# Performance work log

Measured on AMD Instinct MI355X. Metric: run time of the kernel, lower is better.

## Reference

```python
import jax, jax.numpy as jnp
import numpy as np

B, L, D, H = 2, 2048, 1024, 16
HD = D // H
HID = 4 * D
EPS = 1e-5


def setup_inputs() -> dict:
    key = jax.random.key(0)
    ks = jax.random.split(key, 16)
    s = 0.02
    inp = {
        "x": jax.random.normal(ks[0], (B, L, D), jnp.float32),
        "mask": jnp.triu(jnp.ones((L, L), bool), k=1),  # True above diagonal -> masked
        "wq": jax.random.normal(ks[1], (D, D), jnp.float32) * s,
        "wk": jax.random.normal(ks[2], (D, D), jnp.float32) * s,
        "wv": jax.random.normal(ks[3], (D, D), jnp.float32) * s,
        "wo": jax.random.normal(ks[4], (D, D), jnp.float32) * s,
        "ln1_g": jnp.ones((D,), jnp.float32),
        "ln1_b": jnp.zeros((D,), jnp.float32),
        "ln2_g": jnp.ones((D,), jnp.float32),
        "ln2_b": jnp.zeros((D,), jnp.float32),
        "w1": jax.random.normal(ks[5], (HID, D), jnp.float32) * s,
        "b1": jnp.zeros((HID,), jnp.float32),
        "wg": jax.random.normal(ks[6], (HID, D), jnp.float32) * s,
        "w2": jax.random.normal(ks[7], (D, HID), jnp.float32) * s,
        "b2": jnp.zeros((D,), jnp.float32),
    }
    return inp


def _layernorm(x, g, b):
    mu = jnp.mean(x, axis=-1, keepdims=True)
    var = jnp.mean(jnp.square(x - mu), axis=-1, keepdims=True)
    return (x - mu) * jax.lax.rsqrt(var + EPS) * g + b


def _attention(h, mask, wq, wk, wv, wo):
    b, l, d = h.shape
    scale = HD ** -0.5
    # torch Linear: y = x @ W.T (W is [out, in])
    q = (h @ wq.T).reshape(b, l, H, HD)
    k = (h @ wk.T).reshape(b, l, H, HD)
    v = (h @ wv.T).reshape(b, l, H, HD)
    attn = jnp.einsum("bqhd,bkhd->bhqk", q, k) * scale
    attn = jnp.where(mask[None, None, :, :], -jnp.inf, attn)
    pos_bias = jnp.arange(l, dtype=attn.dtype) * 0.01  # additive bias along key axis
    attn = attn + pos_bias[None, None, None, :]
    attn = jax.nn.softmax(attn, axis=-1)
    out = jnp.einsum("bhqk,bkhd->bqhd", attn, v).reshape(b, l, d)
    return out @ wo.T


def _ffn(h, w1, b1, wg, w2, b2):
    return (jax.nn.silu(h @ w1.T + b1) * (h @ wg.T)) @ w2.T + b2


def reference(x, mask, wq, wk, wv, wo, ln1_g, ln1_b, ln2_g, ln2_b, w1, b1, wg, w2, b2):
    x = x + _attention(_layernorm(x, ln1_g, ln1_b), mask, wq, wk, wv, wo)
    x = x + _ffn(_layernorm(x, ln2_g, ln2_b), w1, b1, wg, w2, b2)
    return x
```

## Files before the change

### kernel.cpp

```cpp
#include <hip/hip_runtime.h>

#define ML   2048
#define MD   1024
#define MH   16
#define MHD  64
#define MB   2
#define MM   4096
#define MHID 4096

typedef unsigned short u16;
typedef short bf16x8 __attribute__((ext_vector_type(8)));
typedef float f32x4 __attribute__((ext_vector_type(4)));

__device__ __forceinline__ u16 f2bf(float f) {
    union { float f; unsigned u; } c; c.f = f;
    unsigned r = c.u + 0x7fffu + ((c.u >> 16) & 1u);
    return (u16)(r >> 16);
}
__device__ __forceinline__ float bf2f(u16 h) {
    union { unsigned u; float f; } c; c.u = ((unsigned)h) << 16;
    return c.f;
}

__device__ __forceinline__ int xcd_swz(int orig, int nwg) {
    return (orig & 7) * (nwg >> 3) + (orig >> 3);
}

__device__ __forceinline__ void async_copy16(const u16* g, u16* l) {
    __builtin_amdgcn_global_load_lds(
        (const __attribute__((address_space(1))) void*)g,
        (__attribute__((address_space(3))) void*)l, 16, 0, 0);
}

struct ConvPack {
    const float* src[13];
    u16* dst[13];
    int n[13];
    int start[14];
};

__global__ __launch_bounds__(256)
void conv_all(ConvPack p)
{
    const int bx = blockIdx.x;
    int seg = 0;
    while (seg < 12 && bx >= p.start[seg + 1]) ++seg;
    const int local = bx - p.start[seg];
    const int idx = (local * 256 + threadIdx.x) * 8;
    if (idx >= p.n[seg]) return;
    const float* in = p.src[seg];
    const float4 a = *(const float4*)(in + idx);
    const float4 b = *(const float4*)(in + idx + 4);
    union { bf16x8 v; u16 s[8]; } u;
    u.s[0] = f2bf(a.x); u.s[1] = f2bf(a.y); u.s[2] = f2bf(a.z); u.s[3] = f2bf(a.w);
    u.s[4] = f2bf(b.x); u.s[5] = f2bf(b.y); u.s[6] = f2bf(b.z); u.s[7] = f2bf(b.w);
    *(bf16x8*)&p.dst[seg][idx] = u.v;
}

template<int MI, int NI>
__device__ __forceinline__ void gemm_core(
    const u16* __restrict__ A, const u16* __restrict__ Bm,
    int m0, int n0, int lda, int ldb, int K,
    u16* As, u16* Bs, f32x4 (&acc)[MI][NI])
{
    constexpr int TM = MI * 32;
    constexpr int TN = NI * 32;
    const int tid  = threadIdx.x;
    const int wave = tid >> 6, lane = tid & 63;
    const int wm = wave & 1, wn = wave >> 1;
    const int l15 = lane & 15, quad = lane >> 4;

    const int srow = wave * 16 + (lane >> 2);
    const int scol = (lane & 3) * 8;
    const u16* Ag = A  + (size_t)(m0 + srow) * lda + scol;
    const u16* Bg = Bm + (size_t)(n0 + srow) * ldb + scol;
    u16* Asw = As + srow * 32 + scol;
    u16* Bsw = Bs + srow * 32 + scol;

    f32x4 zero4 = {0.f, 0.f, 0.f, 0.f};
#pragma unroll
    for (int mi = 0; mi < MI; ++mi)
#pragma unroll
        for (int ni = 0; ni < NI; ++ni) acc[mi][ni] = zero4;

    for (int k0 = 0; k0 < K; k0 += 32) {
        __syncthreads();
#pragma unroll
        for (int p = 0; p < TM / 64; ++p)
            async_copy16(Ag + k0 + (size_t)p * 64 * lda, Asw + p * 64 * 32);
#pragma unroll
        for (int p = 0; p < TN / 64; ++p)
            async_copy16(Bg + k0 + (size_t)p * 64 * ldb, Bsw + p * 64 * 32);
        __syncthreads();

        bf16x8 af[MI], bfr[NI];
#pragma unroll
        for (int mi = 0; mi < MI; ++mi)
            af[mi] = *(const bf16x8*)&As[(wm * MI * 16 + mi * 16 + l15) * 32 + quad * 8];
#pragma unroll
        for (int ni = 0; ni < NI; ++ni)
            bfr[ni] = *(const bf16x8*)&Bs[(wn * NI * 16 + ni * 16 + l15) * 32 + quad * 8];
#pragma unroll
        for (int mi = 0; mi < MI; ++mi)
#pragma unroll
            for (int ni = 0; ni < NI; ++ni)
                acc[mi][ni] = __builtin_amdgcn_mfma_f32_16x16x32_bf16(
                    af[mi], bfr[ni], acc[mi][ni], 0, 0, 0);
    }
}

__global__ __launch_bounds__(256)
void ln_kernel(const float* __restrict__ xin,
               const u16* __restrict__ g, const u16* __restrict__ bb,
               u16* __restrict__ out,
               const u16* __restrict__ rbias, float* __restrict__ oinit)
{
    const int row = blockIdx.x;
    const int tid = threadIdx.x;
    const float4 t = *(const float4*)(xin + (size_t)row * MD + tid * 4);
    float v[4] = {t.x, t.y, t.z, t.w};
    if (oinit) {
        const ushort4 rb = *(const ushort4*)&rbias[tid * 4];
        float4 oi;
        oi.x = v[0] + bf2f(rb.x);
        oi.y = v[1] + bf2f(rb.y);
        oi.z = v[2] + bf2f(rb.z);
        oi.w = v[3] + bf2f(rb.w);
        *(float4*)&oinit[(size_t)row * MD + tid * 4] = oi;
    }
    float s  = v[0] + v[1] + v[2] + v[3];
    float s2 = v[0]*v[0] + v[1]*v[1] + v[2]*v[2] + v[3]*v[3];
#pragma unroll
    for (int off = 1; off < 64; off <<= 1) {
        s  += __shfl_xor(s,  off);
        s2 += __shfl_xor(s2, off);
    }
    __shared__ float red[8];
    const int wave = tid >> 6, lane = tid & 63;
    if (lane == 0) { red[wave] = s; red[4 + wave] = s2; }
    __syncthreads();
    s  = red[0] + red[1] + red[2] + red[3];
    s2 = red[4] + red[5] + red[6] + red[7];
    const float mu  = s * (1.0f / MD);
    const float var = fmaxf(s2 * (1.0f / MD) - mu * mu, 0.0f);
    const float rs  = rsqrtf(var + 1e-5f);
    const ushort4 gv = *(const ushort4*)&g[tid * 4];
    const ushort4 bv = *(const ushort4*)&bb[tid * 4];
    ushort4 o;
    o.x = f2bf((v[0] - mu) * rs * bf2f(gv.x) + bf2f(bv.x));
    o.y = f2bf((v[1] - mu) * rs * bf2f(gv.y) + bf2f(bv.y));
    o.z = f2bf((v[2] - mu) * rs * bf2f(gv.z) + bf2f(bv.z));
    o.w = f2bf((v[3] - mu) * rs * bf2f(gv.w) + bf2f(bv.w));
    *(ushort4*)&out[(size_t)row * MD + tid * 4] = o;
}

__global__ __launch_bounds__(256, 2)
void gemm_qkv(const u16* __restrict__ ln, const u16* __restrict__ wq,
              const u16* __restrict__ wk, const u16* __restrict__ wv,
              u16* __restrict__ q, u16* __restrict__ k, u16* __restrict__ vt)
{
    __shared__ __align__(16) u16 As[128 * 32];
    __shared__ __align__(16) u16 Bs[128 * 32];
    const int orig = blockIdx.x + 32 * blockIdx.y + 256 * blockIdx.z;
    const int wid  = xcd_swz(orig, 768);
    const int bx = wid & 31, by = (wid >> 5) & 7, z = wid >> 8;
    const u16* Bm = (z == 0) ? wq : (z == 1) ? wk : wv;
    const int m0 = bx * 128, n0 = by * 128;
    f32x4 acc[4][4];
    gemm_core<4, 4>(ln, Bm, m0, n0, MD, MD, MD, As, Bs, acc);

    const int tid = threadIdx.x;
    const int wave = tid >> 6, lane = tid & 63;
    const int wm = wave & 1, wn = wave >> 1, l15 = lane & 15, quad = lane >> 4;
    if (z < 2) {
        u16* out = (z == 0) ? q : k;
        const float scale = (z == 0) ? 0.125f : 1.0f;
#pragma unroll
        for (int mi = 0; mi < 4; ++mi)
#pragma unroll
            for (int ni = 0; ni < 4; ++ni)
#pragma unroll
                for (int r = 0; r < 4; ++r) {
                    const int row = m0 + wm * 64 + mi * 16 + quad * 4 + r;
                    const int col = n0 + wn * 64 + ni * 16 + l15;
                    out[(size_t)row * MD + col] = f2bf(acc[mi][ni][r] * scale);
                }
    } else {
#pragma unroll
        for (int mi = 0; mi < 4; ++mi)
#pragma unroll
            for (int ni = 0; ni < 4; ++ni) {
                const int row0 = m0 + wm * 64 + mi * 16 + quad * 4;
                const int col  = n0 + wn * 64 + ni * 16 + l15;
                const int bb = row0 >> 11, l = row0 & (ML - 1);
                const int hh = col >> 6,  hd = col & (MHD - 1);
                ushort4 pk;
                pk.x = f2bf(acc[mi][ni][0]);
                pk.y = f2bf(acc[mi][ni][1]);
                pk.z = f2bf(acc[mi][ni][2]);
                pk.w = f2bf(acc[mi][ni][3]);
                *(ushort4*)&vt[((size_t)(bb * MH + hh) * MHD + hd) * ML + l] = pk;
            }
    }
}

__global__ __launch_bounds__(256, 2)
void attn_kernel(const u16* __restrict__ Q, const u16* __restrict__ Kb,
                 const u16* __restrict__ Vt, u16* __restrict__ O)
{
    __shared__ __align__(16) u16 Ks[64 * 64];
    __shared__ __align__(16) u16 Vs[64 * 64];
    __shared__ __align__(16) u16 Pl[4][16 * 72];
    const int tid = threadIdx.x, wave = tid >> 6, lane = tid & 63;
    const int quad = lane >> 4, l15 = lane & 15;
    const int idx = blockIdx.x;
    const int qt = (ML / 64 - 1) - (idx >> 5);
    const int hb = idx & 31;
    const int h = hb & 15, b = hb >> 4;
    const int q0 = qt * 64;
    const int qrow = q0 + wave * 16;
    const float L2E = 1.44269504f;
    const float C1 = 0.01f * L2E;
    const float C2 = -32.0f * L2E;

    u16* Plw = Pl[wave];

    const size_t qoff = ((size_t)(b * ML + qrow + l15)) * MD + h * MHD + quad * 8;
    const bf16x8 aq0 = *(const bf16x8*)&Q[qoff];
    const bf16x8 aq1 = *(const bf16x8*)&Q[qoff + 32];

    const int str = tid >> 3;
    const int sj  = tid & 7;
    const int sjx = (sj ^ (str & 7)) * 8;
    const u16* Kg = Kb + (size_t)(b * ML) * MD + h * MHD;
    const u16* Vg = Vt + (size_t)((b * MH + h) * MHD) * ML;

    const int rsw0 = ((quad    ) ^ (l15 & 7)) * 8;
    const int rsw1 = ((quad + 4) ^ (l15 & 7)) * 8;

    bf16x8 onesf;
    {
        const short v = (l15 == 0) ? (short)0x3F80 : (short)0;
        onesf = (bf16x8){v, v, v, v, v, v, v, v};
    }

    f32x4 zero4 = {0.f, 0.f, 0.f, 0.f};
    f32x4 Oacc[4];
    f32x4 lsum = zero4;
#pragma unroll
    for (int i = 0; i < 4; ++i) Oacc[i] = zero4;

    for (int kt = 0; kt <= qt; ++kt) {
        const int k0 = kt * 64;

        __syncthreads();
        async_copy16(Kg + (size_t)(k0 + str) * MD + sjx,        Ks + tid * 8);
        async_copy16(Kg + (size_t)(k0 + 32 + str) * MD + sjx,   Ks + 2048 + tid * 8);
        async_copy16(Vg + (size_t)str * ML + k0 + sjx,          Vs + tid * 8);
        async_copy16(Vg + (size_t)(32 + str) * ML + k0 + sjx,   Vs + 2048 + tid * 8);
        __syncthreads();

        f32x4 s[4];
#pragma unroll
        for (int jn = 0; jn < 4; ++jn) {
            const int krow = (jn * 16 + l15) * 64;
            const bf16x8 k0f = *(const bf16x8*)&Ks[krow + rsw0];
            const bf16x8 k1f = *(const bf16x8*)&Ks[krow + rsw1];
            f32x4 z = zero4;
            z = __builtin_amdgcn_mfma_f32_16x16x32_bf16(aq0, k0f, z, 0, 0, 0);
            z = __builtin_amdgcn_mfma_f32_16x16x32_bf16(aq1, k1f, z, 0, 0, 0);
            s[jn] = z;
        }

        const bool diag = (kt == qt);
#pragma unroll
        for (int jn = 0; jn < 4; ++jn) {
            const int key = k0 + jn * 16 + l15;
            const float pbm = fmaf((float)key, C1, C2);
#pragma unroll
            for (int r = 0; r < 4; ++r) {
                float val = fmaf(s[jn][r], L2E, pbm);
                if (diag && key > qrow + quad * 4 + r) val = -30000.f;
                union { float f; unsigned u; } c;
                c.f = exp2f(val);
                Plw[(quad * 4 + r) * 72 + jn * 16 + l15] = (u16)(c.u >> 16);
            }
        }

        bf16x8 vv[4][2];
#pragma unroll
        for (int j = 0; j < 4; ++j) {
            const int vrow = (j * 16 + l15) * 64;
            vv[j][0] = *(const bf16x8*)&Vs[vrow + rsw0];
            vv[j][1] = *(const bf16x8*)&Vs[vrow + rsw1];
        }

        const bf16x8 ap0 = *(const bf16x8*)&Plw[l15 * 72 + quad * 8];
        const bf16x8 ap1 = *(const bf16x8*)&Plw[l15 * 72 + 32 + quad * 8];
#pragma unroll
        for (int j = 0; j < 4; ++j) {
            Oacc[j] = __builtin_amdgcn_mfma_f32_16x16x32_bf16(ap0, vv[j][0], Oacc[j], 0, 0, 0);
            Oacc[j] = __builtin_amdgcn_mfma_f32_16x16x32_bf16(ap1, vv[j][1], Oacc[j], 0, 0, 0);
        }
        lsum = __builtin_amdgcn_mfma_f32_16x16x32_bf16(ap0, onesf, lsum, 0, 0, 0);
        lsum = __builtin_amdgcn_mfma_f32_16x16x32_bf16(ap1, onesf, lsum, 0, 0, 0);
    }

#pragma unroll
    for (int r = 0; r < 4; ++r) {
        const float l = __shfl(lsum[r], lane & 48);
        const float inv = 1.0f / l;
        const int row = qrow + quad * 4 + r;
#pragma unroll
        for (int j = 0; j < 4; ++j) {
            const int col = h * MHD + j * 16 + l15;
            O[((size_t)(b * ML + row)) * MD + col] = f2bf(Oacc[j][r] * inv);
        }
    }
}

__global__ __launch_bounds__(256, 2)
void gemm_wo(const u16* __restrict__ ao, const u16* __restrict__ wo,
             const float* __restrict__ x, float* __restrict__ h1)
{
    __shared__ __align__(16) u16 As[64 * 32];
    __shared__ __align__(16) u16 Bs[128 * 32];
    const int orig = blockIdx.x + 64 * blockIdx.y;
    const int wid  = xcd_swz(orig, 512);
    const int m0 = (wid & 63) * 64, n0 = (wid >> 6) * 128;
    f32x4 acc[2][4];
    gemm_core<2, 4>(ao, wo, m0, n0, MD, MD, MD, As, Bs, acc);
    const int tid = threadIdx.x;
    const int wave = tid >> 6, lane = tid & 63;
    const int wm = wave & 1, wn = wave >> 1, l15 = lane & 15, quad = lane >> 4;
#pragma unroll
    for (int mi = 0; mi < 2; ++mi)
#pragma unroll
        for (int ni = 0; ni < 4; ++ni)
#pragma unroll
            for (int r = 0; r < 4; ++r) {
                const int row = m0 + wm * 32 + mi * 16 + quad * 4 + r;
                const int col = n0 + wn * 64 + ni * 16 + l15;
                const size_t idx = (size_t)row * MD + col;
                h1[idx] = acc[mi][ni][r] + x[idx];
            }
}

__global__ __launch_bounds__(512, 2)
void gemm_ug256(const u16* __restrict__ ln, const u16* __restrict__ w1,
                const u16* __restrict__ wg, const u16* __restrict__ b1,
                u16* __restrict__ hf)
{
    __shared__ __align__(16) u16 smem[4][16384];
    const int tid = threadIdx.x;
    const int wave = tid >> 6, lane = tid & 63;
    const int wm = wave >> 2, wn = wave & 3;
    const int l15 = lane & 15, quad = lane >> 4;
    const int orig = blockIdx.x + 16 * blockIdx.y;
    const int wid  = xcd_swz(orig, 512);
    const int m0 = (wid & 15) * 256, n0 = (wid >> 4) * 128;

    const int str = tid >> 3;
    const int sjx = ((tid & 7) ^ (str & 7)) * 8;
    const u16* Ag  = ln + (size_t)(m0 + str) * MD + sjx;
    const u16* B1g = w1 + (size_t)(n0 + str) * MD + sjx;
    const u16* B2g = wg + (size_t)(n0 + str) * MD + sjx;

    f32x4 zero4 = {0.f, 0.f, 0.f, 0.f};
    f32x4 acc[8][4];
#pragma unroll
    for (int mi = 0; mi < 8; ++mi)
#pragma unroll
        for (int ni = 0; ni < 4; ++ni) acc[mi][ni] = zero4;

#define UG_STAGE(d, k0)                                                        \
    do {                                                                       \
        _Pragma("unroll")                                                      \
        for (int p = 0; p < 4; ++p)                                            \
            async_copy16(Ag + (size_t)p * 64 * MD + (k0),                      \
                         &smem[d][p * 4096 + tid * 8]);                        \
        _Pragma("unroll")                                                      \
        for (int p = 0; p < 2; ++p)                                            \
            async_copy16(B1g + (size_t)p * 64 * MD + (k0),                     \
                         &smem[2 + (d)][p * 4096 + tid * 8]);                  \
        _Pragma("unroll")                                                      \
        for (int p = 0; p < 2; ++p)                                            \
            async_copy16(B2g + (size_t)p * 64 * MD + (k0),                     \
                         &smem[2 + (d)][(p + 2) * 4096 + tid * 8]);            \
    } while (0)

    UG_STAGE(0, 0);
    __syncthreads();

    for (int t = 0; t < 16; ++t) {
        const int d = t & 1;
        const u16* Abuf = smem[d];
        const u16* Bbuf = smem[2 + d];

        bf16x8 bfr[4][2], af0[4][2];
#pragma unroll
        for (int ni = 0; ni < 4; ++ni)
#pragma unroll
            for (int kh = 0; kh < 2; ++kh)
                bfr[ni][kh] = *(const bf16x8*)&Bbuf[(wn * 64 + ni * 16 + l15) * 64
                                                    + ((kh * 4 + quad) ^ (l15 & 7)) * 8];
#pragma unroll
        for (int mi = 0; mi < 4; ++mi)
#pragma unroll
            for (int kh = 0; kh < 2; ++kh)
                af0[mi][kh] = *(const bf16x8*)&Abuf[(wm * 128 + mi * 16 + l15) * 64
                                                    + ((kh * 4 + quad) ^ (l15 & 7)) * 8];

        if (t < 15) UG_STAGE(d ^ 1, (t + 1) * 64);

        __builtin_amdgcn_s_setprio(1);
#pragma unroll
        for (int mi = 0; mi < 4; ++mi)
#pragma unroll
            for (int ni = 0; ni < 4; ++ni) {
                acc[mi][ni] = __builtin_amdgcn_mfma_f32_16x16x32_bf16(
                    af0[mi][0], bfr[ni][0], acc[mi][ni], 0, 0, 0);
                acc[mi][ni] = __builtin_amdgcn_mfma_f32_16x16x32_bf16(
                    af0[mi][1], bfr[ni][1], acc[mi][ni], 0, 0, 0);
            }
        __builtin_amdgcn_s_setprio(0);
        __builtin_amdgcn_s_barrier();

        bf16x8 af1[4][2];
#pragma unroll
        for (int mi = 0; mi < 4; ++mi)
#pragma unroll
            for (int kh = 0; kh < 2; ++kh)
                af1[mi][kh] = *(const bf16x8*)&Abuf[(wm * 128 + (mi + 4) * 16 + l15) * 64
                                                    + ((kh * 4 + quad) ^ (l15 & 7)) * 8];
        __builtin_amdgcn_s_setprio(1);
#pragma unroll
        for (int mi = 0; mi < 4; ++mi)
#pragma unroll
            for (int ni = 0; ni < 4; ++ni) {
                acc[mi + 4][ni] = __builtin_amdgcn_mfma_f32_16x16x32_bf16(
                    af1[mi][0], bfr[ni][0], acc[mi + 4][ni], 0, 0, 0);
                acc[mi + 4][ni] = __builtin_amdgcn_mfma_f32_16x16x32_bf16(
                    af1[mi][1], bfr[ni][1], acc[mi + 4][ni], 0, 0, 0);
            }
        __builtin_amdgcn_s_setprio(0);

        __syncthreads();
    }
#undef UG_STAGE

    float* X = (float*)&smem[0][0];
    if (wn < 2) {
        float* Xw = X + (wm * 2 + wn) * 8192;
#pragma unroll
        for (int mi = 0; mi < 8; ++mi)
#pragma unroll
            for (int ni = 0; ni < 4; ++ni)
#pragma unroll
                for (int r = 0; r < 4; ++r)
                    Xw[((mi * 4 + ni) * 4 + r) * 64 + lane] = acc[mi][ni][r];
    }
    __syncthreads();
    if (wn >= 2) {
        const float* Xw = X + (wm * 2 + (wn - 2)) * 8192;
#pragma unroll
        for (int mi = 0; mi < 8; ++mi)
#pragma unroll
            for (int ni = 0; ni < 4; ++ni) {
                const int col = n0 + (wn - 2) * 64 + ni * 16 + l15;
                const float bb1 = bf2f(b1[col]);
#pragma unroll
                for (int r = 0; r < 4; ++r) {
                    const int row = m0 + wm * 128 + mi * 16 + quad * 4 + r;
                    const float uv = Xw[((mi * 4 + ni) * 4 + r) * 64 + lane] + bb1;
                    const float si = uv / (1.0f + __expf(-uv));
                    hf[(size_t)row * MHID + col] = f2bf(si * acc[mi][ni][r]);
                }
            }
    }
}

__global__ __launch_bounds__(256, 2)
void gemm_w2(const u16* __restrict__ hf, const u16* __restrict__ w2,
             float* __restrict__ out)
{
    __shared__ __align__(16) u16 As[128 * 32];
    __shared__ __align__(16) u16 Bs[128 * 32];
    const int orig = blockIdx.x + 32 * blockIdx.y + 256 * blockIdx.z;
    const int wid  = xcd_swz(orig, 512);
    const int m0 = (wid & 31) * 128, n0 = ((wid >> 5) & 7) * 128;
    const int kz = (wid >> 8) * 2048;
    f32x4 acc[4][4];
    gemm_core<4, 4>(hf + kz, w2 + kz, m0, n0, MHID, MHID, 2048, As, Bs, acc);
    const int tid = threadIdx.x;
    const int wave = tid >> 6, lane = tid & 63;
    const int wm = wave & 1, wn = wave >> 1, l15 = lane & 15, quad = lane >> 4;
#pragma unroll
    for (int mi = 0; mi < 4; ++mi)
#pragma unroll
        for (int ni = 0; ni < 4; ++ni)
#pragma unroll
            for (int r = 0; r < 4; ++r) {
                const int row = m0 + wm * 64 + mi * 16 + quad * 4 + r;
                const int col = n0 + wn * 64 + ni * 16 + l15;
                unsafeAtomicAdd(&out[(size_t)row * MD + col], acc[mi][ni][r]);
            }
}

extern "C" void kernel_launch(void* const* d_in, const int* in_sizes, int n_in,
                              void* d_out, int out_size, void* d_ws, size_t ws_size,
                              hipStream_t stream)
{
    const float* x    = (const float*)d_in[0];
    const float* wq   = (const float*)d_in[2];
    const float* wk   = (const float*)d_in[3];
    const float* wv   = (const float*)d_in[4];
    const float* wo   = (const float*)d_in[5];
    const float* ln1g = (const float*)d_in[6];
    const float* ln1b = (const float*)d_in[7];
    const float* ln2g = (const float*)d_in[8];
    const float* ln2b = (const float*)d_in[9];
    const float* w1   = (const float*)d_in[10];
    const float* b1   = (const float*)d_in[11];
    const float* wgp  = (const float*)d_in[12];
    const float* w2   = (const float*)d_in[13];
    const float* b2   = (const float*)d_in[14];
    float* out = (float*)d_out;

    char* ws = (char*)d_ws;
    u16*  wqb  = (u16*)(ws);
    u16*  wkb  = (u16*)(ws + ((size_t)2  << 20));
    u16*  wvb  = (u16*)(ws + ((size_t)4  << 20));
    u16*  wob  = (u16*)(ws + ((size_t)6  << 20));
    u16*  w1b  = (u16*)(ws + ((size_t)8  << 20));
    u16*  wgb  = (u16*)(ws + ((size_t)16 << 20));
    u16*  w2b  = (u16*)(ws + ((size_t)24 << 20));
    char* vec  = ws + ((size_t)32 << 20);
    u16*  l1g  = (u16*)(vec);
    u16*  l1b  = (u16*)(vec + 4096);
    u16*  l2g  = (u16*)(vec + 8192);
    u16*  l2b  = (u16*)(vec + 12288);
    u16*  b1b  = (u16*)(vec + 16384);
    u16*  b2b  = (u16*)(vec + 24576);
    u16*   ln  = (u16*)(ws + ((size_t)33 << 20));
    u16*   q   = (u16*)(ws + ((size_t)41 << 20));
    u16*   k   = (u16*)(ws + ((size_t)49 << 20));
    u16*   vt  = (u16*)(ws + ((size_t)57 << 20));
    u16*   ao  = ln;
    float* h1  = (float*)(ws + ((size_t)41 << 20));
    u16*   hf  = (u16*)(ws + ((size_t)89 << 20));

    const int NW = MD * MD;
    const int NF = MHID * MD;
    ConvPack cp;
    const float* srcs[13] = {wq, wk, wv, wo, w1, wgp, w2, ln1g, ln1b, ln2g, ln2b, b1, b2};
    u16* dsts[13]         = {wqb, wkb, wvb, wob, w1b, wgb, w2b, l1g, l1b, l2g, l2b, b1b, b2b};
    int  ns[13]           = {NW, NW, NW, NW, NF, NF, NF, MD, MD, MD, MD, MHID, MD};
    int start = 0;
    for (int i = 0; i < 13; ++i) {
        cp.src[i] = srcs[i]; cp.dst[i] = dsts[i]; cp.n[i] = ns[i];
        cp.start[i] = start;
        start += (ns[i] + 2047) / 2048;
    }
    cp.start[13] = start;
    conv_all<<<start, 256, 0, stream>>>(cp);

    ln_kernel<<<MM, 256, 0, stream>>>(x, l1g, l1b, ln, nullptr, nullptr);
    gemm_qkv<<<dim3(MM / 128, MD / 128, 3), 256, 0, stream>>>(ln, wqb, wkb, wvb, q, k, vt);
    attn_kernel<<<(ML / 64) * MH * MB, 256, 0, stream>>>(q, k, vt, ao);
    gemm_wo<<<dim3(MM / 64, MD / 128), 256, 0, stream>>>(ao, wob, x, h1);
    ln_kernel<<<MM, 256, 0, stream>>>(h1, l2g, l2b, ln, b2b, out);
    gemm_ug256<<<dim3(MM / 256, MHID / 128), 512, 0, stream>>>(ln, w1b, wgb, b1b, hf);
    gemm_w2<<<dim3(MM / 128, MD / 128, 2), 256, 0, stream>>>(hf, w2b, out);
}
```

Measured before the change: 404.4 us.

## Double-buffer K/V tiles in attention kernel to overlap loads with compute

The attention kernel now keeps two LDS buffers for the K and V tiles. It issues the async copy of the next key tile right after the current K fragments are read into registers, so global-memory latency overlaps with the QK MFMA, softmax and PV work. This also cuts the per-iteration barriers from two to one. The cost is doubled K/V shared memory and more live registers for the K fragments, which could reduce occupancy.

```diff
diff --git a/kernel.cpp b/kernel.cpp
--- a/kernel.cpp
+++ b/kernel.cpp
@@ -208,8 +208,8 @@
 void attn_kernel(const u16* __restrict__ Q, const u16* __restrict__ Kb,
                  const u16* __restrict__ Vt, u16* __restrict__ O)
 {
-    __shared__ __align__(16) u16 Ks[64 * 64];
-    __shared__ __align__(16) u16 Vs[64 * 64];
+    __shared__ __align__(16) u16 Ks[2][64 * 64];
+    __shared__ __align__(16) u16 Vs[2][64 * 64];
     __shared__ __align__(16) u16 Pl[4][16 * 72];
     const int tid = threadIdx.x, wave = tid >> 6, lane = tid & 63;
     const int quad = lane >> 4, l15 = lane & 15;
@@ -250,25 +250,36 @@
 #pragma unroll
     for (int i = 0; i < 4; ++i) Oacc[i] = zero4;
 
+#define ATTN_STAGE(d, k0)                                                      \
+    do {                                                                       \
+        async_copy16(Kg + (size_t)((k0) + str) * MD + sjx,      &Ks[d][tid * 8]);        \
+        async_copy16(Kg + (size_t)((k0) + 32 + str) * MD + sjx, &Ks[d][2048 + tid * 8]); \
+        async_copy16(Vg + (size_t)str * ML + (k0) + sjx,        &Vs[d][tid * 8]);        \
+        async_copy16(Vg + (size_t)(32 + str) * ML + (k0) + sjx, &Vs[d][2048 + tid * 8]); \
+    } while (0)
+
+    ATTN_STAGE(0, 0);
+    __syncthreads();
+
     for (int kt = 0; kt <= qt; ++kt) {
         const int k0 = kt * 64;
-
-        __syncthreads();
-        async_copy16(Kg + (size_t)(k0 + str) * MD + sjx,        Ks + tid * 8);
-        async_copy16(Kg + (size_t)(k0 + 32 + str) * MD + sjx,   Ks + 2048 + tid * 8);
-        async_copy16(Vg + (size_t)str * ML + k0 + sjx,          Vs + tid * 8);
-        async_copy16(Vg + (size_t)(32 + str) * ML + k0 + sjx,   Vs + 2048 + tid * 8);
-        __syncthreads();
-
-        f32x4 s[4];
+        const int d = kt & 1;
+
+        bf16x8 kf[4][2];
 #pragma unroll
         for (int jn = 0; jn < 4; ++jn) {
             const int krow = (jn * 16 + l15) * 64;
-            const bf16x8 k0f = *(const bf16x8*)&Ks[krow + rsw0];
-            const bf16x8 k1f = *(const bf16x8*)&Ks[krow + rsw1];
+            kf[jn][0] = *(const bf16x8*)&Ks[d][krow + rsw0];
+            kf[jn][1] = *(const bf16x8*)&Ks[d][krow + rsw1];
+        }
+        if (kt < qt) ATTN_STAGE(d ^ 1, k0 + 64);
+
+        f32x4 s[4];
+#pragma unroll
+        for (int jn = 0; jn < 4; ++jn) {
             f32x4 z = zero4;
-            z = __builtin_amdgcn_mfma_f32_16x16x32_bf16(aq0, k0f, z, 0, 0, 0);
-            z = __builtin_amdgcn_mfma_f32_16x16x32_bf16(aq1, k1f, z, 0, 0, 0);
+            z = __builtin_amdgcn_mfma_f32_16x16x32_bf16(aq0, kf[jn][0], z, 0, 0, 0);
+            z = __builtin_amdgcn_mfma_f32_16x16x32_bf16(aq1, kf[jn][1], z, 0, 0, 0);
             s[jn] = z;
         }
 
@@ -291,8 +302,8 @@
 #pragma unroll
         for (int j = 0; j < 4; ++j) {
             const int vrow = (j * 16 + l15) * 64;
-            vv[j][0] = *(const bf16x8*)&Vs[vrow + rsw0];
-            vv[j][1] = *(const bf16x8*)&Vs[vrow + rsw1];
+            vv[j][0] = *(const bf16x8*)&Vs[d][vrow + rsw0];
+            vv[j][1] = *(const bf16x8*)&Vs[d][vrow + rsw1];
         }
 
         const bf16x8 ap0 = *(const bf16x8*)&Plw[l15 * 72 + quad * 8];
@@ -304,7 +315,10 @@
         }
         lsum = __builtin_amdgcn_mfma_f32_16x16x32_bf16(ap0, onesf, lsum, 0, 0, 0);
         lsum = __builtin_amdgcn_mfma_f32_16x16x32_bf16(ap1, onesf, lsum, 0, 0, 0);
-    }
+
+        __syncthreads();
+    }
+#undef ATTN_STAGE
 
 #pragma unroll
     for (int r = 0; r < 4; ++r) {
```

Result: no change. 401.0 us (-0.8%).
